# Optimization experiments

Hardware: AMD Instinct MI355X
Metric: run time of the kernel (lower is better)

## Reference

```python
import jax, jax.numpy as jnp
import numpy as np

SEQ_LEN = 4096
HIDDEN = 1280
NUM_HEADS = 16
HEAD_DIM = HIDDEN // NUM_HEADS  # 80
NUM_SEQS = 8


def setup_inputs() -> dict:
    key = jax.random.key(0)
    ks = jax.random.split(key, 8)
    x = jax.random.normal(ks[0], (SEQ_LEN, HIDDEN), dtype=jnp.float32)
    # rotary tables: use cos/sin of random angles so they are bounded like real RoPE tables
    ang = jax.random.uniform(ks[1], (SEQ_LEN, HEAD_DIM), dtype=jnp.float32) * 6.283185
    cos = jnp.cos(ang)
    sin = jnp.sin(ang)
    # variable-length packed segments: strictly increasing boundaries incl. 0 and SEQ_LEN
    rng = np.random.default_rng(0)
    inner = np.sort(rng.choice(np.arange(1, SEQ_LEN), size=NUM_SEQS - 1, replace=False))
    cu_seqlens = jnp.asarray(np.concatenate([[0], inner, [SEQ_LEN]]), dtype=jnp.int32)
    s = 0.02
    w_qkv = jax.random.normal(ks[2], (HIDDEN, 3 * HIDDEN), dtype=jnp.float32) * s
    b_qkv = jnp.zeros((3 * HIDDEN,), dtype=jnp.float32)
    w_proj = jax.random.normal(ks[3], (HIDDEN, HIDDEN), dtype=jnp.float32) * s
    b_proj = jnp.zeros((HIDDEN,), dtype=jnp.float32)
    return {"x": x, "cu_seqlens": cu_seqlens, "cos": cos, "sin": sin,
            "w_qkv": w_qkv, "b_qkv": b_qkv, "w_proj": w_proj, "b_proj": b_proj}


def _rotate_half(t):
    d = t.shape[-1] // 2
    return jnp.concatenate([-t[..., d:], t[..., :d]], axis=-1)


def _apply_rope(q, k, cos, sin):
    # q,k: (S,H,D); cos,sin: (S,D) broadcast over heads, computed in fp32
    c = cos[:, None, :].astype(jnp.float32)
    s = sin[:, None, :].astype(jnp.float32)
    qf, kf = q.astype(jnp.float32), k.astype(jnp.float32)
    q_out = qf * c + _rotate_half(qf) * s
    k_out = kf * c + _rotate_half(kf) * s
    return q_out.astype(q.dtype), k_out.astype(k.dtype)


def reference(x, cu_seqlens, cos, sin, w_qkv, b_qkv, w_proj, b_proj):
    S = x.shape[0]
    scale = HEAD_DIM ** (-0.5)
    qkv = (x @ w_qkv + b_qkv).reshape(S, 3, NUM_HEADS, HEAD_DIM)
    q, k, v = qkv[:, 0], qkv[:, 1], qkv[:, 2]  # each (S,H,D)
    q, k = _apply_rope(q, k, cos, sin)
    # block-diagonal varlen attention via segment-id mask (same math as per-chunk softmax)
    pos = jnp.arange(S)
    seg = jnp.searchsorted(cu_seqlens[1:], pos, side='right')  # (S,) segment id
    mask = seg[:, None] == seg[None, :]  # (S,S) block-diagonal
    scores = jnp.einsum('shd,thd->hst', q, k) * scale  # (H,S,S)
    scores = jnp.where(mask[None], scores.astype(jnp.float32), jnp.finfo(jnp.float32).min)
    attn = jax.nn.softmax(scores, axis=-1).astype(q.dtype)
    out = jnp.einsum('hst,thd->shd', attn, v).reshape(S, NUM_HEADS * HEAD_DIM)
    return out @ w_proj + b_proj
```

## Files before the change

kernel.cpp:

```cpp
#include <hip/hip_runtime.h>
#include <cstdint>
#include <cstddef>

typedef __bf16 bf16x8 __attribute__((ext_vector_type(8)));
typedef float f32x4 __attribute__((ext_vector_type(4)));

#define SEQ   4096
#define HID   1280
#define NH    16
#define HD    80

__device__ __forceinline__ unsigned short f2bf(float f) {
  unsigned int u = __float_as_uint(f);
  unsigned int r = u + 0x7FFFu + ((u >> 16) & 1u);
  return (unsigned short)(r >> 16);
}
__device__ __forceinline__ float bf2f(unsigned short h) {
  return __uint_as_float(((unsigned int)h) << 16);
}
__device__ __forceinline__ __bf16 us2bf(unsigned short u) {
  union { unsigned short s; __bf16 b; } c; c.s = u; return c.b;
}
__device__ __forceinline__ void dma16(const void* g, void* l) {
  __builtin_amdgcn_global_load_lds((const __attribute__((address_space(1))) unsigned int*)g,
                                   (__attribute__((address_space(3))) unsigned int*)l, 16, 0, 0);
}

__global__ __launch_bounds__(256) void split_kernel(const float* __restrict__ x,
                                                    unsigned short* __restrict__ hi,
                                                    unsigned short* __restrict__ lo,
                                                    int n4) {
  int i = blockIdx.x * 256 + threadIdx.x;
  if (i >= n4) return;
  float4 v = *((const float4*)x + i);
  float vv[4] = {v.x, v.y, v.z, v.w};
  unsigned short hh[4], ll[4];
#pragma unroll
  for (int j = 0; j < 4; ++j) {
    hh[j] = f2bf(vv[j]);
    ll[j] = f2bf(vv[j] - bf2f(hh[j]));
  }
  *((ushort4*)hi + i) = make_ushort4(hh[0], hh[1], hh[2], hh[3]);
  *((ushort4*)lo + i) = make_ushort4(ll[0], ll[1], ll[2], ll[3]);
}

__global__ __launch_bounds__(256) void tsplit_kernel(const float* __restrict__ W,
                                                     unsigned short* __restrict__ Thi,
                                                     unsigned short* __restrict__ Tlo,
                                                     int K, int N) {
  __shared__ float tile[32][33];
  int n0 = blockIdx.x * 32, k0 = blockIdx.y * 32;
  int tx = threadIdx.x & 31, ty = threadIdx.x >> 5;
#pragma unroll
  for (int i = 0; i < 32; i += 8)
    tile[ty + i][tx] = W[(size_t)(k0 + ty + i) * N + n0 + tx];
  __syncthreads();
#pragma unroll
  for (int i = 0; i < 32; i += 8) {
    float v = tile[tx][ty + i];
    size_t idx = (size_t)(n0 + ty + i) * K + (size_t)(k0 + tx);
    unsigned short h = f2bf(v);
    Thi[idx] = h;
    Tlo[idx] = f2bf(v - bf2f(h));
  }
}

__global__ __launch_bounds__(256, 2) void gemm128_x3(
    const unsigned short* __restrict__ Ah, const unsigned short* __restrict__ Al,
    const unsigned short* __restrict__ Bh, const unsigned short* __restrict__ Bl,
    const float* __restrict__ bias,
    float* __restrict__ out0, float* __restrict__ out1, float* __restrict__ out2,
    int M, int N, int K) {
  __shared__ __align__(16) unsigned short sT[4][8192];

  const int t = threadIdx.x;
  const int lane = t & 63, wave = t >> 6;
  const int c16 = lane & 15, quad = lane >> 4;
  const int bm = blockIdx.y * 128, bn = blockIdx.x * 128;
  const int wr = (wave >> 1) * 64, wc = (wave & 1) * 64;

  f32x4 acc[4][4];
#pragma unroll
  for (int i = 0; i < 4; ++i)
#pragma unroll
    for (int j = 0; j < 4; ++j) acc[i][j] = (f32x4){0.f, 0.f, 0.f, 0.f};

  const int lrow = lane >> 3;
  const int lswz = (lane & 7) ^ lrow;
  const unsigned short* garr = (wave == 0) ? Ah : (wave == 1) ? Al
                               : (wave == 2) ? Bh : Bl;
  const int gbase_row = (wave < 2) ? bm : bn;
  unsigned short* larr = &sT[wave][0];

  for (int k0 = 0; k0 < K; k0 += 64) {
    __syncthreads();
#pragma unroll
    for (int i = 0; i < 16; ++i) {
      const unsigned short* g = garr + (size_t)(gbase_row + 8 * i + lrow) * K
                                + k0 + lswz * 8;
      dma16(g, larr + i * 512);
    }
    __syncthreads();
#pragma unroll
    for (int ks = 0; ks < 2; ++ks) {
      const int aswz = ((ks * 4 + quad) ^ (c16 & 7)) * 8;
      bf16x8 a[4][2], b[4][2];
#pragma unroll
      for (int mi = 0; mi < 4; ++mi) {
        int row = wr + mi * 16 + c16;
        a[mi][0] = *(const bf16x8*)&sT[0][row * 64 + aswz];
        a[mi][1] = *(const bf16x8*)&sT[1][row * 64 + aswz];
      }
#pragma unroll
      for (int ni = 0; ni < 4; ++ni) {
        int row = wc + ni * 16 + c16;
        b[ni][0] = *(const bf16x8*)&sT[2][row * 64 + aswz];
        b[ni][1] = *(const bf16x8*)&sT[3][row * 64 + aswz];
      }
#pragma unroll
      for (int mi = 0; mi < 4; ++mi)
#pragma unroll
        for (int ni = 0; ni < 4; ++ni) {
          acc[mi][ni] = __builtin_amdgcn_mfma_f32_16x16x32_bf16(a[mi][0], b[ni][0], acc[mi][ni], 0, 0, 0);
          acc[mi][ni] = __builtin_amdgcn_mfma_f32_16x16x32_bf16(a[mi][0], b[ni][1], acc[mi][ni], 0, 0, 0);
          acc[mi][ni] = __builtin_amdgcn_mfma_f32_16x16x32_bf16(a[mi][1], b[ni][0], acc[mi][ni], 0, 0, 0);
        }
    }
  }
#pragma unroll
  for (int ni = 0; ni < 4; ++ni) {
    int colg = bn + wc + ni * 16 + c16;
    float bv = bias[colg];
    float* op;
    int c = colg;
    if (c < 1280) op = out0;
    else if (c < 2560) { op = out1; c -= 1280; }
    else { op = out2; c -= 2560; }
#pragma unroll
    for (int mi = 0; mi < 4; ++mi) {
#pragma unroll
      for (int r = 0; r < 4; ++r) {
        int rowg = bm + wr + mi * 16 + quad * 4 + r;
        op[(size_t)rowg * 1280 + c] = acc[mi][ni][r] + bv;
      }
    }
  }
}

__global__ __launch_bounds__(256) void rope_pack_kernel(
    float* __restrict__ qf, const float* __restrict__ kf,
    const float* __restrict__ cs, const float* __restrict__ sn,
    unsigned short* __restrict__ khi, unsigned short* __restrict__ klo) {
  const int h = blockIdx.y;
  const int s = blockIdx.x * 64 + (threadIdx.x >> 2);
  const int p = threadIdx.x & 3;
  float* qrow = qf + (size_t)s * HID + h * HD;
  const float* krow = kf + (size_t)s * HID + h * HD;
  const float* cr = cs + (size_t)s * HD;
  const float* sr = sn + (size_t)s * HD;
  unsigned short* kh = khi + ((size_t)h * SEQ + s) * HD;
  unsigned short* kl = klo + ((size_t)h * SEQ + s) * HD;
#pragma unroll
  for (int j = 0; j < 10; ++j) {
    int d = 10 * p + j;
    float c0 = cr[d], s0 = sr[d], c1 = cr[d + 40], s1 = sr[d + 40];
    float q0 = qrow[d], q1 = qrow[d + 40];
    qrow[d]      = q0 * c0 - q1 * s0;
    qrow[d + 40] = q1 * c1 + q0 * s1;
    float k0 = krow[d], k1 = krow[d + 40];
    float kn0 = k0 * c0 - k1 * s0;
    float kn1 = k1 * c1 + k0 * s1;
    unsigned short h0 = f2bf(kn0), h1 = f2bf(kn1);
    kh[d] = h0;      kl[d] = f2bf(kn0 - bf2f(h0));
    kh[d + 40] = h1; kl[d + 40] = f2bf(kn1 - bf2f(h1));
  }
}

__global__ __launch_bounds__(256) void vt_pack_kernel(const float* __restrict__ vf,
                                                      unsigned short* __restrict__ vthi,
                                                      unsigned short* __restrict__ vtlo) {
  __shared__ unsigned short sTh[80][72];
  __shared__ unsigned short sTl[80][72];
  const int h = blockIdx.y;
  const int s0 = blockIdx.x * 64;
  const int t = threadIdx.x;
  {
    int row = t >> 2, p = (t & 3) * 20;
    const float* src = vf + (size_t)(s0 + row) * HID + h * HD + p;
#pragma unroll
    for (int i = 0; i < 5; ++i) {
      float4 v = *(const float4*)(src + 4 * i);
      float vv[4] = {v.x, v.y, v.z, v.w};
#pragma unroll
      for (int j = 0; j < 4; ++j) {
        int d = p + 4 * i + j;
        unsigned short hu = f2bf(vv[j]);
        sTh[d][row] = hu;
        sTl[d][row] = f2bf(vv[j] - bf2f(hu));
      }
    }
  }
  __syncthreads();
  if (t < 160) {
    int d = t >> 1, half = (t & 1) * 32;
    size_t base = (size_t)(h * HD + d) * SEQ + s0 + half;
#pragma unroll
    for (int i = 0; i < 8; ++i) {
      *(ushort4*)&vthi[base + 4 * i] = *(ushort4*)&sTh[d][half + 4 * i];
      *(ushort4*)&vtlo[base + 4 * i] = *(ushort4*)&sTl[d][half + 4 * i];
    }
  }
}

__global__ __launch_bounds__(256, 2) void attn_kernel(
    const float* __restrict__ qf, const unsigned short* __restrict__ khi,
    const unsigned short* __restrict__ klo, const unsigned short* __restrict__ vthi,
    const unsigned short* __restrict__ vtlo, const int* __restrict__ cu,
    unsigned short* __restrict__ ohi, unsigned short* __restrict__ olo) {
  __shared__ __align__(16) unsigned short sKh[64 * 80];
  __shared__ __align__(16) unsigned short sKl[64 * 80];
  __shared__ __align__(16) unsigned short sVh[80 * 64];
  __shared__ __align__(16) unsigned short sVl[80 * 64];
  __shared__ __align__(16) unsigned int   sP[64][68];
  __shared__ int segk[64], segq[64];
  __shared__ int cu_s[9];

  const int t = threadIdx.x;
  const int h = blockIdx.x;
  const int r0 = blockIdx.y * 64;
  const int lane = t & 63, wave = t >> 6;
  const int c16 = lane & 15, quad = lane >> 4;

  if (t < 9) cu_s[t] = cu[t];
  __syncthreads();
  if (t < 64) {
    int pos = r0 + t, sg = 0;
#pragma unroll
    for (int i = 1; i < 8; ++i) sg += (pos >= cu_s[i]) ? 1 : 0;
    segq[t] = sg;
  }
  __syncthreads();
  const int kstart = cu_s[segq[0]];
  const int kend   = cu_s[segq[63] + 1];
  const int ck0    = kstart & ~63;
  int sq[4];
#pragma unroll
  for (int r = 0; r < 4; ++r) sq[r] = segq[wave * 16 + quad * 4 + r];

  const float scale = 0.11180339887498949f;
  bf16x8 qh[3], ql[3];
  {
    const float* qrow = qf + (size_t)(r0 + wave * 16 + c16) * HID + h * HD;
#pragma unroll
    for (int ks = 0; ks < 3; ++ks) {
      int d = ks * 32 + quad * 8;
      bf16x8 hf = {}, lf = {};
      if (d < 80) {
        float4 v0 = *(const float4*)(qrow + d);
        float4 v1 = *(const float4*)(qrow + d + 4);
        float vv[8] = {v0.x, v0.y, v0.z, v0.w, v1.x, v1.y, v1.z, v1.w};
#pragma unroll
        for (int j = 0; j < 8; ++j) {
          float v = vv[j] * scale;
          unsigned short hu = f2bf(v);
          hf[j] = us2bf(hu);
          lf[j] = us2bf(f2bf(v - bf2f(hu)));
        }
      }
      qh[ks] = hf; ql[ks] = lf;
    }
  }

  f32x4 O[5];
#pragma unroll
  for (int dt = 0; dt < 5; ++dt) O[dt] = (f32x4){0.f, 0.f, 0.f, 0.f};
  float mrow[4] = {-1e30f, -1e30f, -1e30f, -1e30f};
  float lrow[4] = {0.f, 0.f, 0.f, 0.f};

  const int lr8 = lane >> 3;
  const int vswz_dma = (lane & 7) ^ lr8;

  for (int ck = ck0; ck < kend; ck += 64) {
    __syncthreads();
    if (wave < 2) {
      const unsigned short* garr = wave ? klo : khi;
      unsigned short* larr = wave ? sKl : sKh;
      size_t base = ((size_t)h * SEQ + ck) * 80;
#pragma unroll
      for (int i = 0; i < 10; ++i)
        dma16(garr + base + i * 512 + lane * 8, larr + i * 512);
    } else {
      const unsigned short* garr = (wave == 3) ? vtlo : vthi;
      unsigned short* larr = (wave == 3) ? sVl : sVh;
#pragma unroll
      for (int i = 0; i < 10; ++i)
        dma16(garr + (size_t)(h * HD + 8 * i + lr8) * SEQ + ck + vswz_dma * 8,
              larr + i * 512);
    }
    if (t < 64) {
      int tk = ck + t, sg = -1;
      if (tk < kend) {
        sg = 0;
#pragma unroll
        for (int i = 1; i < 8; ++i) sg += (tk >= cu_s[i]) ? 1 : 0;
      }
      segk[t] = sg;
    }
    __syncthreads();

    f32x4 sc[4];
#pragma unroll
    for (int nt = 0; nt < 4; ++nt) sc[nt] = (f32x4){0.f, 0.f, 0.f, 0.f};
#pragma unroll
    for (int nt = 0; nt < 4; ++nt) {
      int krow = nt * 16 + c16;
#pragma unroll
      for (int ks = 0; ks < 3; ++ks) {
        int d = ks * 32 + quad * 8;
        bf16x8 kh = {}, kl = {};
        if (d < 80) {
          kh = *(const bf16x8*)&sKh[krow * 80 + d];
          kl = *(const bf16x8*)&sKl[krow * 80 + d];
        }
        sc[nt] = __builtin_amdgcn_mfma_f32_16x16x32_bf16(qh[ks], kh, sc[nt], 0, 0, 0);
        sc[nt] = __builtin_amdgcn_mfma_f32_16x16x32_bf16(qh[ks], kl, sc[nt], 0, 0, 0);
        sc[nt] = __builtin_amdgcn_mfma_f32_16x16x32_bf16(ql[ks], kh, sc[nt], 0, 0, 0);
      }
    }

    int sk[4];
#pragma unroll
    for (int nt = 0; nt < 4; ++nt) sk[nt] = segk[nt * 16 + c16];
    float alpha[4];
#pragma unroll
    for (int r = 0; r < 4; ++r) {
      float mx = -1e30f;
#pragma unroll
      for (int nt = 0; nt < 4; ++nt) {
        float v = (sk[nt] == sq[r]) ? sc[nt][r] : -1e30f;
        mx = fmaxf(mx, v);
      }
      mx = fmaxf(mx, __shfl_xor(mx, 1));
      mx = fmaxf(mx, __shfl_xor(mx, 2));
      mx = fmaxf(mx, __shfl_xor(mx, 4));
      mx = fmaxf(mx, __shfl_xor(mx, 8));
      float mnew = fmaxf(mrow[r], mx);
      alpha[r] = __expf(mrow[r] - mnew);
      float ps = 0.f;
#pragma unroll
      for (int nt = 0; nt < 4; ++nt) {
        float p = (sk[nt] == sq[r]) ? __expf(sc[nt][r] - mnew) : 0.f;
        ps += p;
        unsigned short ph = f2bf(p);
        unsigned short pl = f2bf(p - bf2f(ph));
        sP[wave * 16 + quad * 4 + r][nt * 16 + c16] = (unsigned)ph | ((unsigned)pl << 16);
      }
      ps += __shfl_xor(ps, 1);
      ps += __shfl_xor(ps, 2);
      ps += __shfl_xor(ps, 4);
      ps += __shfl_xor(ps, 8);
      lrow[r] = lrow[r] * alpha[r] + ps;
      mrow[r] = mnew;
    }
#pragma unroll
    for (int dt = 0; dt < 5; ++dt) {
      f32x4 ov = O[dt];
      ov[0] *= alpha[0]; ov[1] *= alpha[1]; ov[2] *= alpha[2]; ov[3] *= alpha[3];
      O[dt] = ov;
    }
    __syncthreads();

#pragma unroll
    for (int ks = 0; ks < 2; ++ks) {
      uint4 w0 = *(const uint4*)&sP[wave * 16 + c16][ks * 32 + quad * 8];
      uint4 w1 = *(const uint4*)&sP[wave * 16 + c16][ks * 32 + quad * 8 + 4];
      union { unsigned int u[4]; bf16x8 v; } ph, pl;
      ph.u[0] = __builtin_amdgcn_perm(w0.y, w0.x, 0x05040100u);
      ph.u[1] = __builtin_amdgcn_perm(w0.w, w0.z, 0x05040100u);
      ph.u[2] = __builtin_amdgcn_perm(w1.y, w1.x, 0x05040100u);
      ph.u[3] = __builtin_amdgcn_perm(w1.w, w1.z, 0x05040100u);
      pl.u[0] = __builtin_amdgcn_perm(w0.y, w0.x, 0x07060302u);
      pl.u[1] = __builtin_amdgcn_perm(w0.w, w0.z, 0x07060302u);
      pl.u[2] = __builtin_amdgcn_perm(w1.y, w1.x, 0x07060302u);
      pl.u[3] = __builtin_amdgcn_perm(w1.w, w1.z, 0x07060302u);
      const int g = ks * 4 + quad;
#pragma unroll
      for (int dt = 0; dt < 5; ++dt) {
        int d = dt * 16 + c16;
        int off = d * 64 + ((g ^ (d & 7)) * 8);
        bf16x8 vh = *(const bf16x8*)&sVh[off];
        bf16x8 vl = *(const bf16x8*)&sVl[off];
        O[dt] = __builtin_amdgcn_mfma_f32_16x16x32_bf16(ph.v, vh, O[dt], 0, 0, 0);
        O[dt] = __builtin_amdgcn_mfma_f32_16x16x32_bf16(ph.v, vl, O[dt], 0, 0, 0);
        O[dt] = __builtin_amdgcn_mfma_f32_16x16x32_bf16(pl.v, vh, O[dt], 0, 0, 0);
      }
    }
  }

  float inv[4];
#pragma unroll
  for (int r = 0; r < 4; ++r) inv[r] = 1.0f / lrow[r];
#pragma unroll
  for (int dt = 0; dt < 5; ++dt)
#pragma unroll
    for (int r = 0; r < 4; ++r) {
      int rowg = r0 + wave * 16 + quad * 4 + r;
      float val = O[dt][r] * inv[r];
      unsigned short hu = f2bf(val);
      size_t idx = (size_t)rowg * HID + h * HD + dt * 16 + c16;
      ohi[idx] = hu;
      olo[idx] = f2bf(val - bf2f(hu));
    }
}

extern "C" void kernel_launch(void* const* d_in, const int* in_sizes, int n_in,
                              void* d_out, int out_size, void* d_ws, size_t ws_size,
                              hipStream_t stream) {
  const float* x      = (const float*)d_in[0];
  const int*   cu     = (const int*)d_in[1];
  const float* cs     = (const float*)d_in[2];
  const float* sn     = (const float*)d_in[3];
  const float* w_qkv  = (const float*)d_in[4];
  const float* b_qkv  = (const float*)d_in[5];
  const float* w_proj = (const float*)d_in[6];
  const float* b_proj = (const float*)d_in[7];
  float* out = (float*)d_out;

  char* ws = (char*)d_ws;
  float*          qf     = (float*)(ws + 0);
  float*          kf     = (float*)(ws + 20971520ULL);
  float*          vf     = (float*)(ws + 41943040ULL);
  unsigned short* o_hi   = (unsigned short*)(ws + 20971520ULL);
  unsigned short* o_lo   = (unsigned short*)(ws + 31457280ULL);
  unsigned short* wpt_hi = (unsigned short*)(ws + 41943040ULL);
  unsigned short* wpt_lo = (unsigned short*)(ws + 45219840ULL);
  unsigned short* x_hi   = (unsigned short*)(ws + 62914560ULL);
  unsigned short* x_lo   = (unsigned short*)(ws + 73400320ULL);
  unsigned short* khi    = (unsigned short*)(ws + 62914560ULL);
  unsigned short* klo    = (unsigned short*)(ws + 73400320ULL);
  unsigned short* wqt_hi = (unsigned short*)(ws + 83886080ULL);
  unsigned short* wqt_lo = (unsigned short*)(ws + 93716480ULL);
  unsigned short* vthi   = (unsigned short*)(ws + 83886080ULL);
  unsigned short* vtlo   = (unsigned short*)(ws + 94371840ULL);

  split_kernel<<<5120, 256, 0, stream>>>(x, x_hi, x_lo, 1310720);
  tsplit_kernel<<<dim3(120, 40), 256, 0, stream>>>(w_qkv, wqt_hi, wqt_lo, 1280, 3840);
  gemm128_x3<<<dim3(30, 32), 256, 0, stream>>>(x_hi, x_lo, wqt_hi, wqt_lo,
                                               b_qkv, qf, kf, vf, 4096, 3840, 1280);
  rope_pack_kernel<<<dim3(64, 16), 256, 0, stream>>>(qf, kf, cs, sn, khi, klo);
  vt_pack_kernel<<<dim3(64, 16), 256, 0, stream>>>(vf, vthi, vtlo);
  tsplit_kernel<<<dim3(40, 40), 256, 0, stream>>>(w_proj, wpt_hi, wpt_lo, 1280, 1280);
  attn_kernel<<<dim3(16, 64), 256, 0, stream>>>(qf, khi, klo, vthi, vtlo, cu, o_hi, o_lo);
  gemm128_x3<<<dim3(10, 32), 256, 0, stream>>>(o_hi, o_lo, wpt_hi, wpt_lo,
                                               b_proj, out, nullptr, nullptr, 4096, 1280, 1280);
}
```

Baseline: 457.2 us.

## Drop activation low-part splits, persistent atomic-scheduled attention with register P and prefetch

Activations (x and the attention output) now keep only a bf16 high part, so both GEMMs run two bf16 MFMAs per tile instead of three and split_kernel writes a single array. Attention becomes a persistent kernel: blocks pull (head, row-block) work items from an atomic counter that vt_pack_kernel resets. P is redistributed across lanes with ds_bpermute instead of going through shared memory, segment masks are computed from per-row bounds, and K/V chunk loads are issued for the next chunk while the current one is being processed. Occupancy hints are raised to three blocks per CU, and the workspace layout is reshuffled. The goal is less MFMA and memory work, but dropping the activation low parts lowers accuracy relative to the fp32 reference.

Result: faster. 412.6 us (-9.8%).

```diff
diff --git a/kernel.cpp b/kernel.cpp
--- a/kernel.cpp
+++ b/kernel.cpp
@@ -26,22 +26,13 @@
                                    (__attribute__((address_space(3))) unsigned int*)l, 16, 0, 0);
 }
 
-__global__ __launch_bounds__(256) void split_kernel(const float* __restrict__ x,
-                                                    unsigned short* __restrict__ hi,
-                                                    unsigned short* __restrict__ lo,
-                                                    int n4) {
+__global__ __launch_bounds__(256) void split_hi_kernel(const float* __restrict__ x,
+                                                       unsigned short* __restrict__ hi,
+                                                       int n4) {
   int i = blockIdx.x * 256 + threadIdx.x;
   if (i >= n4) return;
   float4 v = *((const float4*)x + i);
-  float vv[4] = {v.x, v.y, v.z, v.w};
-  unsigned short hh[4], ll[4];
-#pragma unroll
-  for (int j = 0; j < 4; ++j) {
-    hh[j] = f2bf(vv[j]);
-    ll[j] = f2bf(vv[j] - bf2f(hh[j]));
-  }
-  *((ushort4*)hi + i) = make_ushort4(hh[0], hh[1], hh[2], hh[3]);
-  *((ushort4*)lo + i) = make_ushort4(ll[0], ll[1], ll[2], ll[3]);
+  *((ushort4*)hi + i) = make_ushort4(f2bf(v.x), f2bf(v.y), f2bf(v.z), f2bf(v.w));
 }
 
 __global__ __launch_bounds__(256) void tsplit_kernel(const float* __restrict__ W,
@@ -65,65 +56,65 @@
   }
 }
 
-__global__ __launch_bounds__(256, 2) void gemm128_x3(
-    const unsigned short* __restrict__ Ah, const unsigned short* __restrict__ Al,
-    const unsigned short* __restrict__ Bh, const unsigned short* __restrict__ Bl,
-    const float* __restrict__ bias,
+__global__ __launch_bounds__(256, 3) void gemm128_x2(
+    const unsigned short* __restrict__ A, const unsigned short* __restrict__ Bh,
+    const unsigned short* __restrict__ Bl, const float* __restrict__ bias,
     float* __restrict__ out0, float* __restrict__ out1, float* __restrict__ out2,
     int M, int N, int K) {
-  __shared__ __align__(16) unsigned short sT[4][8192];
+  __shared__ __align__(16) unsigned short sALL[3 * 8192];
 
   const int t = threadIdx.x;
   const int lane = t & 63, wave = t >> 6;
   const int c16 = lane & 15, quad = lane >> 4;
   const int bm = blockIdx.y * 128, bn = blockIdx.x * 128;
   const int wr = (wave >> 1) * 64, wc = (wave & 1) * 64;
-
-  f32x4 acc[4][4];
-#pragma unroll
-  for (int i = 0; i < 4; ++i)
-#pragma unroll
-    for (int j = 0; j < 4; ++j) acc[i][j] = (f32x4){0.f, 0.f, 0.f, 0.f};
-
   const int lrow = lane >> 3;
   const int lswz = (lane & 7) ^ lrow;
-  const unsigned short* garr = (wave == 0) ? Ah : (wave == 1) ? Al
-                               : (wave == 2) ? Bh : Bl;
-  const int gbase_row = (wave < 2) ? bm : bn;
-  unsigned short* larr = &sT[wave][0];
+
+  f32x4 acc[4][4];
+#pragma unroll
+  for (int i = 0; i < 4; ++i)
+#pragma unroll
+    for (int j = 0; j < 4; ++j) acc[i][j] = (f32x4){0.f, 0.f, 0.f, 0.f};
+
+  const unsigned short* gp[12];
+#pragma unroll
+  for (int i = 0; i < 12; ++i) {
+    const int ua = wave * 12 + i;
+    const int arr = ua >> 4, sub = ua & 15;
+    const unsigned short* g = (arr == 0) ? A : (arr == 1) ? Bh : Bl;
+    const int rowg = ((arr == 0) ? bm : bn) + sub * 8 + lrow;
+    gp[i] = g + (size_t)rowg * K + lswz * 8;
+  }
 
   for (int k0 = 0; k0 < K; k0 += 64) {
     __syncthreads();
 #pragma unroll
-    for (int i = 0; i < 16; ++i) {
-      const unsigned short* g = garr + (size_t)(gbase_row + 8 * i + lrow) * K
-                                + k0 + lswz * 8;
-      dma16(g, larr + i * 512);
-    }
+    for (int i = 0; i < 12; ++i)
+      dma16(gp[i] + k0, &sALL[(wave * 12 + i) * 512]);
     __syncthreads();
 #pragma unroll
     for (int ks = 0; ks < 2; ++ks) {
-      const int aswz = ((ks * 4 + quad) ^ (c16 & 7)) * 8;
-      bf16x8 a[4][2], b[4][2];
+      bf16x8 a[4], bh[4], bl[4];
 #pragma unroll
       for (int mi = 0; mi < 4; ++mi) {
-        int row = wr + mi * 16 + c16;
-        a[mi][0] = *(const bf16x8*)&sT[0][row * 64 + aswz];
-        a[mi][1] = *(const bf16x8*)&sT[1][row * 64 + aswz];
+        const int row = wr + mi * 16 + c16;
+        const int off = row * 64 + (((ks * 4 + quad) ^ (row & 7)) * 8);
+        a[mi] = *(const bf16x8*)&sALL[off];
       }
 #pragma unroll
       for (int ni = 0; ni < 4; ++ni) {
-        int row = wc + ni * 16 + c16;
-        b[ni][0] = *(const bf16x8*)&sT[2][row * 64 + aswz];
-        b[ni][1] = *(const bf16x8*)&sT[3][row * 64 + aswz];
+        const int row = wc + ni * 16 + c16;
+        const int off = row * 64 + (((ks * 4 + quad) ^ (row & 7)) * 8);
+        bh[ni] = *(const bf16x8*)&sALL[8192 + off];
+        bl[ni] = *(const bf16x8*)&sALL[16384 + off];
       }
 #pragma unroll
       for (int mi = 0; mi < 4; ++mi)
 #pragma unroll
         for (int ni = 0; ni < 4; ++ni) {
-          acc[mi][ni] = __builtin_amdgcn_mfma_f32_16x16x32_bf16(a[mi][0], b[ni][0], acc[mi][ni], 0, 0, 0);
-          acc[mi][ni] = __builtin_amdgcn_mfma_f32_16x16x32_bf16(a[mi][0], b[ni][1], acc[mi][ni], 0, 0, 0);
-          acc[mi][ni] = __builtin_amdgcn_mfma_f32_16x16x32_bf16(a[mi][1], b[ni][0], acc[mi][ni], 0, 0, 0);
+          acc[mi][ni] = __builtin_amdgcn_mfma_f32_16x16x32_bf16(a[mi], bh[ni], acc[mi][ni], 0, 0, 0);
+          acc[mi][ni] = __builtin_amdgcn_mfma_f32_16x16x32_bf16(a[mi], bl[ni], acc[mi][ni], 0, 0, 0);
         }
     }
   }
@@ -137,13 +128,12 @@
     else if (c < 2560) { op = out1; c -= 1280; }
     else { op = out2; c -= 2560; }
 #pragma unroll
-    for (int mi = 0; mi < 4; ++mi) {
+    for (int mi = 0; mi < 4; ++mi)
 #pragma unroll
       for (int r = 0; r < 4; ++r) {
         int rowg = bm + wr + mi * 16 + quad * 4 + r;
         op[(size_t)rowg * 1280 + c] = acc[mi][ni][r] + bv;
       }
-    }
   }
 }
 
@@ -178,7 +168,9 @@
 
 __global__ __launch_bounds__(256) void vt_pack_kernel(const float* __restrict__ vf,
                                                       unsigned short* __restrict__ vthi,
-                                                      unsigned short* __restrict__ vtlo) {
+                                                      unsigned short* __restrict__ vtlo,
+                                                      unsigned int* __restrict__ ctr) {
+  if (blockIdx.x == 0 && blockIdx.y == 0 && threadIdx.x == 0) *ctr = 0u;
   __shared__ unsigned short sTh[80][72];
   __shared__ unsigned short sTl[80][72];
   const int h = blockIdx.y;
@@ -212,205 +204,225 @@
   }
 }
 
-__global__ __launch_bounds__(256, 2) void attn_kernel(
+__global__ __launch_bounds__(256, 3) void attn_kernel(
     const float* __restrict__ qf, const unsigned short* __restrict__ khi,
     const unsigned short* __restrict__ klo, const unsigned short* __restrict__ vthi,
     const unsigned short* __restrict__ vtlo, const int* __restrict__ cu,
-    unsigned short* __restrict__ ohi, unsigned short* __restrict__ olo) {
-  __shared__ __align__(16) unsigned short sKh[64 * 80];
-  __shared__ __align__(16) unsigned short sKl[64 * 80];
-  __shared__ __align__(16) unsigned short sVh[80 * 64];
-  __shared__ __align__(16) unsigned short sVl[80 * 64];
-  __shared__ __align__(16) unsigned int   sP[64][68];
-  __shared__ int segk[64], segq[64];
+    unsigned short* __restrict__ ohi, unsigned int* __restrict__ ctr) {
+  __shared__ __align__(16) unsigned short sKh[5120], sKl[5120];
+  __shared__ __align__(16) unsigned short sVh[5120], sVl[5120];
   __shared__ int cu_s[9];
+  __shared__ unsigned int s_u;
 
   const int t = threadIdx.x;
-  const int h = blockIdx.x;
-  const int r0 = blockIdx.y * 64;
   const int lane = t & 63, wave = t >> 6;
   const int c16 = lane & 15, quad = lane >> 4;
+  const int lr8 = lane >> 3;
+  const int vswz = (lane & 7) ^ lr8;
+  const int addrA = ((((2 * quad) & 3) * 16) + c16) << 2;
+  const int addrB = ((((2 * quad + 1) & 3) * 16) + c16) << 2;
 
   if (t < 9) cu_s[t] = cu[t];
-  __syncthreads();
-  if (t < 64) {
-    int pos = r0 + t, sg = 0;
-#pragma unroll
-    for (int i = 1; i < 8; ++i) sg += (pos >= cu_s[i]) ? 1 : 0;
-    segq[t] = sg;
-  }
-  __syncthreads();
-  const int kstart = cu_s[segq[0]];
-  const int kend   = cu_s[segq[63] + 1];
-  const int ck0    = kstart & ~63;
-  int sq[4];
-#pragma unroll
-  for (int r = 0; r < 4; ++r) sq[r] = segq[wave * 16 + quad * 4 + r];
-
-  const float scale = 0.11180339887498949f;
-  bf16x8 qh[3], ql[3];
-  {
-    const float* qrow = qf + (size_t)(r0 + wave * 16 + c16) * HID + h * HD;
-#pragma unroll
-    for (int ks = 0; ks < 3; ++ks) {
-      int d = ks * 32 + quad * 8;
-      bf16x8 hf = {}, lf = {};
-      if (d < 80) {
-        float4 v0 = *(const float4*)(qrow + d);
-        float4 v1 = *(const float4*)(qrow + d + 4);
-        float vv[8] = {v0.x, v0.y, v0.z, v0.w, v1.x, v1.y, v1.z, v1.w};
+
+  for (;;) {
+    __syncthreads();
+    if (t == 0) s_u = atomicAdd(ctr, 1u);
+    __syncthreads();
+    const unsigned int u = s_u;
+    if (u >= 1024u) break;
+    const int h = (int)(u >> 6);
+    const int r0 = (int)(u & 63u) * 64;
+
+    const int q_my = r0 + wave * 16 + c16;
+    int sq = 0, sg0 = 0, sg1 = 0;
+#pragma unroll
+    for (int i = 1; i < 8; ++i) {
+      sq  += (q_my    >= cu_s[i]) ? 1 : 0;
+      sg0 += (r0      >= cu_s[i]) ? 1 : 0;
+      sg1 += (r0 + 63 >= cu_s[i]) ? 1 : 0;
+    }
+    const int kb_lo = cu_s[sq], kb_hi = cu_s[sq + 1];
+    const int ck0 = cu_s[sg0] & ~63;
+    const int kend = cu_s[sg1 + 1];
+    const int nchunk = (kend - ck0 + 63) >> 6;
+
+    const float qsc = 0.11180339887498949f;
+    bf16x8 qh[3], ql[3];
+    {
+      const float* qrow = qf + (size_t)q_my * HID + h * HD;
+#pragma unroll
+      for (int ks = 0; ks < 3; ++ks) {
+        const int d = ks * 32 + quad * 8;
+        bf16x8 hf = {}, lf = {};
+        if (d < 80) {
+          float4 v0 = *(const float4*)(qrow + d);
+          float4 v1 = *(const float4*)(qrow + d + 4);
+          float vv[8] = {v0.x, v0.y, v0.z, v0.w, v1.x, v1.y, v1.z, v1.w};
+#pragma unroll
+          for (int j = 0; j < 8; ++j) {
+            float v = vv[j] * qsc;
+            unsigned short hu = f2bf(v);
+            hf[j] = us2bf(hu);
+            lf[j] = us2bf(f2bf(v - bf2f(hu)));
+          }
+        }
+        qh[ks] = hf; ql[ks] = lf;
+      }
+    }
+
+    f32x4 O[5];
+#pragma unroll
+    for (int dt = 0; dt < 5; ++dt) O[dt] = (f32x4){0.f, 0.f, 0.f, 0.f};
+    float m_i = -1e30f, l_i = 0.f;
+
+    {
+      const unsigned short* gk = (wave & 2) ? klo : khi;
+      unsigned short* lk = ((wave & 2) ? sKl : sKh) + (wave & 1) * 2560;
+      const size_t kb = ((size_t)h * SEQ + ck0) * 80 + (size_t)(wave & 1) * 2560 + lane * 8;
+#pragma unroll
+      for (int i2 = 0; i2 < 5; ++i2) dma16(gk + kb + i2 * 512, lk + i2 * 512);
+      const unsigned short* gv = (wave & 2) ? vtlo : vthi;
+      unsigned short* lv = (wave & 2) ? sVl : sVh;
+      const int u0 = (wave & 1) * 5;
+#pragma unroll
+      for (int i2 = 0; i2 < 5; ++i2) {
+        const int uu = u0 + i2;
+        dma16(gv + (size_t)(h * HD + 8 * uu + lr8) * SEQ + ck0 + vswz * 8, lv + uu * 512);
+      }
+    }
+    __syncthreads();
+
+    for (int ci = 0; ci < nchunk; ++ci) {
+      const int ck = ck0 + ci * 64;
+      f32x4 sc[4];
+#pragma unroll
+      for (int nt = 0; nt < 4; ++nt) sc[nt] = (f32x4){0.f, 0.f, 0.f, 0.f};
+#pragma unroll
+      for (int nt = 0; nt < 4; ++nt) {
+        const int krow = nt * 16 + c16;
+#pragma unroll
+        for (int ks = 0; ks < 3; ++ks) {
+          const int d = ks * 32 + quad * 8;
+          bf16x8 kh = {}, kl = {};
+          if (d < 80) {
+            kh = *(const bf16x8*)&sKh[krow * 80 + d];
+            kl = *(const bf16x8*)&sKl[krow * 80 + d];
+          }
+          sc[nt] = __builtin_amdgcn_mfma_f32_16x16x32_bf16(kh, qh[ks], sc[nt], 0, 0, 0);
+          sc[nt] = __builtin_amdgcn_mfma_f32_16x16x32_bf16(kh, ql[ks], sc[nt], 0, 0, 0);
+          sc[nt] = __builtin_amdgcn_mfma_f32_16x16x32_bf16(kl, qh[ks], sc[nt], 0, 0, 0);
+        }
+      }
+      float mx = -1e30f;
+#pragma unroll
+      for (int nt = 0; nt < 4; ++nt)
+#pragma unroll
+        for (int r = 0; r < 4; ++r) {
+          const int kg = ck + nt * 16 + quad * 4 + r;
+          const bool ok = (kg >= kb_lo) && (kg < kb_hi);
+          float v = ok ? sc[nt][r] : -1e30f;
+          sc[nt][r] = v;
+          mx = fmaxf(mx, v);
+        }
+      mx = fmaxf(mx, __shfl_xor(mx, 16));
+      mx = fmaxf(mx, __shfl_xor(mx, 32));
+      const float mnew = fmaxf(m_i, mx);
+      const float alpha = __expf(m_i - mnew);
+      float ps = 0.f;
+      unsigned int pk[4][4];
+#pragma unroll
+      for (int nt = 0; nt < 4; ++nt)
+#pragma unroll
+        for (int r = 0; r < 4; ++r) {
+          const float s = sc[nt][r];
+          const float p = (s > -1e29f) ? __expf(s - mnew) : 0.f;
+          ps += p;
+          const unsigned int pu = __float_as_uint(p);
+          const unsigned short ph = (unsigned short)(pu >> 16);
+          const unsigned short pl = f2bf(p - bf2f(ph));
+          pk[nt][r] = (unsigned int)ph | ((unsigned int)pl << 16);
+        }
+      ps += __shfl_xor(ps, 16);
+      ps += __shfl_xor(ps, 32);
+      l_i = l_i * alpha + ps;
+      m_i = mnew;
+      float aR[4];
+#pragma unroll
+      for (int r = 0; r < 4; ++r)
+        aR[r] = __uint_as_float((unsigned)__builtin_amdgcn_ds_bpermute(
+                    (quad * 4 + r) << 2, __float_as_int(alpha)));
+#pragma unroll
+      for (int dt = 0; dt < 5; ++dt) {
+        f32x4 o = O[dt];
+        o[0] *= aR[0]; o[1] *= aR[1]; o[2] *= aR[2]; o[3] *= aR[3];
+        O[dt] = o;
+      }
+      __syncthreads();
+      if (ci + 1 < nchunk) {
+        const unsigned short* gk = (wave & 2) ? klo : khi;
+        unsigned short* lk = ((wave & 2) ? sKl : sKh) + (wave & 1) * 2560;
+        const size_t kb = ((size_t)h * SEQ + ck + 64) * 80 + (size_t)(wave & 1) * 2560 + lane * 8;
+#pragma unroll
+        for (int i2 = 0; i2 < 5; ++i2) dma16(gk + kb + i2 * 512, lk + i2 * 512);
+      }
+#pragma unroll
+      for (int ks = 0; ks < 2; ++ks) {
+        unsigned int vj[8];
 #pragma unroll
         for (int j = 0; j < 8; ++j) {
-          float v = vv[j] * scale;
-          unsigned short hu = f2bf(v);
-          hf[j] = us2bf(hu);
-          lf[j] = us2bf(f2bf(v - bf2f(hu)));
-        }
-      }
-      qh[ks] = hf; ql[ks] = lf;
-    }
-  }
-
-  f32x4 O[5];
-#pragma unroll
-  for (int dt = 0; dt < 5; ++dt) O[dt] = (f32x4){0.f, 0.f, 0.f, 0.f};
-  float mrow[4] = {-1e30f, -1e30f, -1e30f, -1e30f};
-  float lrow[4] = {0.f, 0.f, 0.f, 0.f};
-
-  const int lr8 = lane >> 3;
-  const int vswz_dma = (lane & 7) ^ lr8;
-
-  for (int ck = ck0; ck < kend; ck += 64) {
-    __syncthreads();
-    if (wave < 2) {
-      const unsigned short* garr = wave ? klo : khi;
-      unsigned short* larr = wave ? sKl : sKh;
-      size_t base = ((size_t)h * SEQ + ck) * 80;
-#pragma unroll
-      for (int i = 0; i < 10; ++i)
-        dma16(garr + base + i * 512 + lane * 8, larr + i * 512);
-    } else {
-      const unsigned short* garr = (wave == 3) ? vtlo : vthi;
-      unsigned short* larr = (wave == 3) ? sVl : sVh;
-#pragma unroll
-      for (int i = 0; i < 10; ++i)
-        dma16(garr + (size_t)(h * HD + 8 * i + lr8) * SEQ + ck + vswz_dma * 8,
-              larr + i * 512);
-    }
-    if (t < 64) {
-      int tk = ck + t, sg = -1;
-      if (tk < kend) {
-        sg = 0;
-#pragma unroll
-        for (int i = 1; i < 8; ++i) sg += (tk >= cu_s[i]) ? 1 : 0;
-      }
-      segk[t] = sg;
-    }
-    __syncthreads();
-
-    f32x4 sc[4];
-#pragma unroll
-    for (int nt = 0; nt < 4; ++nt) sc[nt] = (f32x4){0.f, 0.f, 0.f, 0.f};
-#pragma unroll
-    for (int nt = 0; nt < 4; ++nt) {
-      int krow = nt * 16 + c16;
-#pragma unroll
-      for (int ks = 0; ks < 3; ++ks) {
-        int d = ks * 32 + quad * 8;
-        bf16x8 kh = {}, kl = {};
-        if (d < 80) {
-          kh = *(const bf16x8*)&sKh[krow * 80 + d];
-          kl = *(const bf16x8*)&sKl[krow * 80 + d];
-        }
-        sc[nt] = __builtin_amdgcn_mfma_f32_16x16x32_bf16(qh[ks], kh, sc[nt], 0, 0, 0);
-        sc[nt] = __builtin_amdgcn_mfma_f32_16x16x32_bf16(qh[ks], kl, sc[nt], 0, 0, 0);
-        sc[nt] = __builtin_amdgcn_mfma_f32_16x16x32_bf16(ql[ks], kh, sc[nt], 0, 0, 0);
-      }
-    }
-
-    int sk[4];
-#pragma unroll
-    for (int nt = 0; nt < 4; ++nt) sk[nt] = segk[nt * 16 + c16];
-    float alpha[4];
-#pragma unroll
-    for (int r = 0; r < 4; ++r) {
-      float mx = -1e30f;
-#pragma unroll
-      for (int nt = 0; nt < 4; ++nt) {
-        float v = (sk[nt] == sq[r]) ? sc[nt][r] : -1e30f;
-        mx = fmaxf(mx, v);
-      }
-      mx = fmaxf(mx, __shfl_xor(mx, 1));
-      mx = fmaxf(mx, __shfl_xor(mx, 2));
-      mx = fmaxf(mx, __shfl_xor(mx, 4));
-      mx = fmaxf(mx, __shfl_xor(mx, 8));
-      float mnew = fmaxf(mrow[r], mx);
-      alpha[r] = __expf(mrow[r] - mnew);
-      float ps = 0.f;
-#pragma unroll
-      for (int nt = 0; nt < 4; ++nt) {
-        float p = (sk[nt] == sq[r]) ? __expf(sc[nt][r] - mnew) : 0.f;
-        ps += p;
-        unsigned short ph = f2bf(p);
-        unsigned short pl = f2bf(p - bf2f(ph));
-        sP[wave * 16 + quad * 4 + r][nt * 16 + c16] = (unsigned)ph | ((unsigned)pl << 16);
-      }
-      ps += __shfl_xor(ps, 1);
-      ps += __shfl_xor(ps, 2);
-      ps += __shfl_xor(ps, 4);
-      ps += __shfl_xor(ps, 8);
-      lrow[r] = lrow[r] * alpha[r] + ps;
-      mrow[r] = mnew;
-    }
-#pragma unroll
-    for (int dt = 0; dt < 5; ++dt) {
-      f32x4 ov = O[dt];
-      ov[0] *= alpha[0]; ov[1] *= alpha[1]; ov[2] *= alpha[2]; ov[3] *= alpha[3];
-      O[dt] = ov;
-    }
-    __syncthreads();
-
-#pragma unroll
-    for (int ks = 0; ks < 2; ++ks) {
-      uint4 w0 = *(const uint4*)&sP[wave * 16 + c16][ks * 32 + quad * 8];
-      uint4 w1 = *(const uint4*)&sP[wave * 16 + c16][ks * 32 + quad * 8 + 4];
-      union { unsigned int u[4]; bf16x8 v; } ph, pl;
-      ph.u[0] = __builtin_amdgcn_perm(w0.y, w0.x, 0x05040100u);
-      ph.u[1] = __builtin_amdgcn_perm(w0.w, w0.z, 0x05040100u);
-      ph.u[2] = __builtin_amdgcn_perm(w1.y, w1.x, 0x05040100u);
-      ph.u[3] = __builtin_amdgcn_perm(w1.w, w1.z, 0x05040100u);
-      pl.u[0] = __builtin_amdgcn_perm(w0.y, w0.x, 0x07060302u);
-      pl.u[1] = __builtin_amdgcn_perm(w0.w, w0.z, 0x07060302u);
-      pl.u[2] = __builtin_amdgcn_perm(w1.y, w1.x, 0x07060302u);
-      pl.u[3] = __builtin_amdgcn_perm(w1.w, w1.z, 0x07060302u);
-      const int g = ks * 4 + quad;
-#pragma unroll
-      for (int dt = 0; dt < 5; ++dt) {
-        int d = dt * 16 + c16;
-        int off = d * 64 + ((g ^ (d & 7)) * 8);
-        bf16x8 vh = *(const bf16x8*)&sVh[off];
-        bf16x8 vl = *(const bf16x8*)&sVl[off];
-        O[dt] = __builtin_amdgcn_mfma_f32_16x16x32_bf16(ph.v, vh, O[dt], 0, 0, 0);
-        O[dt] = __builtin_amdgcn_mfma_f32_16x16x32_bf16(ph.v, vl, O[dt], 0, 0, 0);
-        O[dt] = __builtin_amdgcn_mfma_f32_16x16x32_bf16(pl.v, vh, O[dt], 0, 0, 0);
-      }
-    }
-  }
-
-  float inv[4];
-#pragma unroll
-  for (int r = 0; r < 4; ++r) inv[r] = 1.0f / lrow[r];
-#pragma unroll
-  for (int dt = 0; dt < 5; ++dt)
-#pragma unroll
-    for (int r = 0; r < 4; ++r) {
-      int rowg = r0 + wave * 16 + quad * 4 + r;
-      float val = O[dt][r] * inv[r];
-      unsigned short hu = f2bf(val);
-      size_t idx = (size_t)rowg * HID + h * HD + dt * 16 + c16;
-      ohi[idx] = hu;
-      olo[idx] = f2bf(val - bf2f(hu));
-    }
+          const int addr = (j < 4) ? addrA : addrB;
+          const int r = j & 3;
+          const int v0 = __builtin_amdgcn_ds_bpermute(addr, (int)pk[2 * ks + 0][r]);
+          const int v1 = __builtin_amdgcn_ds_bpermute(addr, (int)pk[2 * ks + 1][r]);
+          vj[j] = (unsigned int)((quad & 2) ? v1 : v0);
+        }
+        union { unsigned int w[4]; bf16x8 v; } ph, pl;
+        ph.w[0] = __builtin_amdgcn_perm(vj[1], vj[0], 0x05040100u);
+        ph.w[1] = __builtin_amdgcn_perm(vj[3], vj[2], 0x05040100u);
+        ph.w[2] = __builtin_amdgcn_perm(vj[5], vj[4], 0x05040100u);
+        ph.w[3] = __builtin_amdgcn_perm(vj[7], vj[6], 0x05040100u);
+        pl.w[0] = __builtin_amdgcn_perm(vj[1], vj[0], 0x07060302u);
+        pl.w[1] = __builtin_amdgcn_perm(vj[3], vj[2], 0x07060302u);
+        pl.w[2] = __builtin_amdgcn_perm(vj[5], vj[4], 0x07060302u);
+        pl.w[3] = __builtin_amdgcn_perm(vj[7], vj[6], 0x07060302u);
+        const int g = ks * 4 + quad;
+#pragma unroll
+        for (int dt = 0; dt < 5; ++dt) {
+          const int d = dt * 16 + c16;
+          const int off = d * 64 + ((g ^ (d & 7)) * 8);
+          bf16x8 vh = *(const bf16x8*)&sVh[off];
+          bf16x8 vl = *(const bf16x8*)&sVl[off];
+          O[dt] = __builtin_amdgcn_mfma_f32_16x16x32_bf16(ph.v, vh, O[dt], 0, 0, 0);
+          O[dt] = __builtin_amdgcn_mfma_f32_16x16x32_bf16(ph.v, vl, O[dt], 0, 0, 0);
+          O[dt] = __builtin_amdgcn_mfma_f32_16x16x32_bf16(pl.v, vh, O[dt], 0, 0, 0);
+        }
+      }
+      __syncthreads();
+      if (ci + 1 < nchunk) {
+        const unsigned short* gv = (wave & 2) ? vtlo : vthi;
+        unsigned short* lv = (wave & 2) ? sVl : sVh;
+        const int u0 = (wave & 1) * 5;
+#pragma unroll
+        for (int i2 = 0; i2 < 5; ++i2) {
+          const int uu = u0 + i2;
+          dma16(gv + (size_t)(h * HD + 8 * uu + lr8) * SEQ + (ck + 64) + vswz * 8, lv + uu * 512);
+        }
+      }
+    }
+    const float inv = 1.0f / l_i;
+    float iR[4];
+#pragma unroll
+    for (int r = 0; r < 4; ++r)
+      iR[r] = __uint_as_float((unsigned)__builtin_amdgcn_ds_bpermute(
+                  (quad * 4 + r) << 2, __float_as_int(inv)));
+#pragma unroll
+    for (int dt = 0; dt < 5; ++dt)
+#pragma unroll
+      for (int r = 0; r < 4; ++r) {
+        const int rowg = r0 + wave * 16 + quad * 4 + r;
+        ohi[(size_t)rowg * HID + h * HD + dt * 16 + c16] = f2bf(O[dt][r] * iR[r]);
+      }
+  }
 }
 
 extern "C" void kernel_launch(void* const* d_in, const int* in_sizes, int n_in,
@@ -429,28 +441,27 @@
   char* ws = (char*)d_ws;
   float*          qf     = (float*)(ws + 0);
   float*          kf     = (float*)(ws + 20971520ULL);
+  unsigned short* vthi   = (unsigned short*)(ws + 20971520ULL);
+  unsigned short* vtlo   = (unsigned short*)(ws + 31457280ULL);
   float*          vf     = (float*)(ws + 41943040ULL);
-  unsigned short* o_hi   = (unsigned short*)(ws + 20971520ULL);
-  unsigned short* o_lo   = (unsigned short*)(ws + 31457280ULL);
-  unsigned short* wpt_hi = (unsigned short*)(ws + 41943040ULL);
-  unsigned short* wpt_lo = (unsigned short*)(ws + 45219840ULL);
+  unsigned short* o_hi   = (unsigned short*)(ws + 41943040ULL);
   unsigned short* x_hi   = (unsigned short*)(ws + 62914560ULL);
-  unsigned short* x_lo   = (unsigned short*)(ws + 73400320ULL);
   unsigned short* khi    = (unsigned short*)(ws + 62914560ULL);
   unsigned short* klo    = (unsigned short*)(ws + 73400320ULL);
   unsigned short* wqt_hi = (unsigned short*)(ws + 83886080ULL);
   unsigned short* wqt_lo = (unsigned short*)(ws + 93716480ULL);
-  unsigned short* vthi   = (unsigned short*)(ws + 83886080ULL);
-  unsigned short* vtlo   = (unsigned short*)(ws + 94371840ULL);
-
-  split_kernel<<<5120, 256, 0, stream>>>(x, x_hi, x_lo, 1310720);
+  unsigned short* wpt_hi = (unsigned short*)(ws + 103546880ULL);
+  unsigned short* wpt_lo = (unsigned short*)(ws + 106823680ULL);
+  unsigned int*   ctr    = (unsigned int*)(ws + 83886080ULL);
+
+  split_hi_kernel<<<5120, 256, 0, stream>>>(x, x_hi, 1310720);
   tsplit_kernel<<<dim3(120, 40), 256, 0, stream>>>(w_qkv, wqt_hi, wqt_lo, 1280, 3840);
-  gemm128_x3<<<dim3(30, 32), 256, 0, stream>>>(x_hi, x_lo, wqt_hi, wqt_lo,
-                                               b_qkv, qf, kf, vf, 4096, 3840, 1280);
+  tsplit_kernel<<<dim3(40, 40), 256, 0, stream>>>(w_proj, wpt_hi, wpt_lo, 1280, 1280);
+  gemm128_x2<<<dim3(30, 32), 256, 0, stream>>>(x_hi, wqt_hi, wqt_lo, b_qkv,
+                                               qf, kf, vf, 4096, 3840, 1280);
   rope_pack_kernel<<<dim3(64, 16), 256, 0, stream>>>(qf, kf, cs, sn, khi, klo);
-  vt_pack_kernel<<<dim3(64, 16), 256, 0, stream>>>(vf, vthi, vtlo);
-  tsplit_kernel<<<dim3(40, 40), 256, 0, stream>>>(w_proj, wpt_hi, wpt_lo, 1280, 1280);
-  attn_kernel<<<dim3(16, 64), 256, 0, stream>>>(qf, khi, klo, vthi, vtlo, cu, o_hi, o_lo);
-  gemm128_x3<<<dim3(10, 32), 256, 0, stream>>>(o_hi, o_lo, wpt_hi, wpt_lo,
-                                               b_proj, out, nullptr, nullptr, 4096, 1280, 1280);
-}
+  vt_pack_kernel<<<dim3(64, 16), 256, 0, stream>>>(vf, vthi, vtlo, ctr);
+  attn_kernel<<<768, 256, 0, stream>>>(qf, khi, klo, vthi, vtlo, cu, o_hi, ctr);
+  gemm128_x2<<<dim3(10, 32), 256, 0, stream>>>(o_hi, wpt_hi, wpt_lo, b_proj,
+                                               out, nullptr, nullptr, 4096, 1280, 1280);
+}
```
